# Kernel tuning notes

Hardware: AMD Instinct MI355X
Metric: run time of the kernel (lower is better)

The kernel has to match this reference:

```python
import jax, jax.numpy as jnp
import numpy as np

ROT_DELTA = 1  # rotation_delta from __init__
BN_EPS = 1e-3  # keras BatchNormalization default epsilon


def conv_dirac(signal, bc_idx, bc_w, W, b):
    """Template-based intrinsic mesh conv (dirac patch operator).

    signal: [N, D]; bc_idx/bc_w: [N, Rr, A, 3]; W: [T, Rr, A, D]; b: [T].
    Returns [N, K, T] with K = A // ROT_DELTA rotations.
    """
    gathered = signal[bc_idx]  # [N, Rr, A, 3, D] irregular gather
    interp = jnp.einsum('vrai,vraid->vrad', bc_w, gathered)  # barycentric interp
    A = interp.shape[2]
    rots = np.arange(0, A, ROT_DELTA)
    # Rotating the (small) template weights is equivalent to rolling the
    # interpolated signal along the angular axis, but far cheaper.
    W_rot = jnp.stack([jnp.roll(W, int(r), axis=2) for r in rots])  # [K, T, Rr, A, D]
    return jnp.einsum('vrad,ktrad->vkt', interp, W_rot) + b  # [N, K, T]


def angular_max_pool(x):
    # Select, per vertex, the rotation whose response has maximal L2 norm.
    k = jnp.argmax(jnp.linalg.norm(x, axis=-1), axis=1)  # [N]
    return jnp.take_along_axis(x, k[:, None, None], axis=1)[:, 0]  # [N, T]


def batch_norm(x, gamma, beta):
    mu = jnp.mean(x, axis=0, keepdims=True)
    var = jnp.var(x, axis=0, keepdims=True)
    return gamma * (x - mu) * jax.lax.rsqrt(var + BN_EPS) + beta


def setup_inputs() -> dict:
    key = jax.random.key(0)
    ks = jax.random.split(key, 6)
    N, Rr, A, D, T = 80000, 5, 8, 32, 32
    signal = jax.random.normal(ks[0], (N, D), dtype=jnp.float32)
    bc_idx = jax.random.randint(ks[1], (N, Rr, A, 3), 0, N)
    bc_w = jax.random.uniform(ks[2], (N, Rr, A, 3), dtype=jnp.float32)
    bc_w = bc_w / jnp.sum(bc_w, axis=-1, keepdims=True)  # barycentric coords sum to 1
    W1 = jax.random.normal(ks[3], (T, Rr, A, D), dtype=jnp.float32) * 0.05
    W2 = jax.random.normal(ks[4], (T, Rr, A, D), dtype=jnp.float32) * 0.05
    return {
        'signal': signal, 'bc_idx': bc_idx, 'bc_w': bc_w,
        'W1': W1, 'b1': jnp.zeros((T,), jnp.float32),
        'gamma1': jnp.ones((T,), jnp.float32), 'beta1': jnp.zeros((T,), jnp.float32),
        'W2': W2, 'b2': jnp.zeros((T,), jnp.float32),
        'gamma2': jnp.ones((T,), jnp.float32), 'beta2': jnp.zeros((T,), jnp.float32),
    }


def reference(signal, bc_idx, bc_w, W1, b1, gamma1, beta1, W2, b2, gamma2, beta2):
    # Branch 1: conv -> angular max-pool -> BN -> relu
    s = conv_dirac(signal, bc_idx, bc_w, W1, b1)
    s = angular_max_pool(s)
    s = batch_norm(s, gamma1, beta1)
    s = jax.nn.relu(s)
    # Branch 2: conv -> angular max-pool -> BN
    s = conv_dirac(s, bc_idx, bc_w, W2, b2)
    s = angular_max_pool(s)
    s = batch_norm(s, gamma2, beta2)
    # Residual add (input_dim == amt_templates -> no rescale branch) + activation
    return jax.nn.relu(s + signal)
```

## Files before the change

kernel.cpp:

```cpp
#include <hip/hip_runtime.h>
#include <math.h>

#define RR 5
#define AA 8
#define DD 32
#define TT 32
#define KK 8

#define RT2 0.70710678118654752f

typedef float v2f __attribute__((ext_vector_type(2)));
typedef float v4f __attribute__((ext_vector_type(4)));

static __device__ __forceinline__ v2f pkfma(v2f a, v2f b, v2f c) {
#if __has_builtin(__builtin_elementwise_fma)
    return __builtin_elementwise_fma(a, b, c);
#else
    v2f r; r.x = fmaf(a.x, b.x, c.x); r.y = fmaf(a.y, b.y, c.y); return r;
#endif
}

__global__ void wdft_kernel(const float* __restrict__ W, float* __restrict__ Ws) {
    int idx = blockIdx.x * 256 + threadIdx.x;
    if (idx >= TT * RR * DD) return;
    int d = idx & 31;
    int tr = idx >> 5;
    int t = tr / 5;
    int r = tr - t * 5;
    float xa[8];
    #pragma unroll
    for (int a = 0; a < 8; ++a) xa[a] = W[(tr * 8 + a) * 32 + d];
    float s0 = xa[0] + xa[4], d0 = xa[0] - xa[4];
    float s1 = xa[1] + xa[5], d1 = xa[1] - xa[5];
    float s2 = xa[2] + xa[6], d2 = xa[2] - xa[6];
    float s3 = xa[3] + xa[7], d3 = xa[3] - xa[7];
    float s02 = s0 + s2, s13 = s1 + s3;
    float F0 = s02 + s13, F4 = s02 - s13;
    float R2 = s0 - s2, I2 = s3 - s1;
    float u = RT2 * (d1 - d3), v = RT2 * (d1 + d3);
    float R1 = d0 + u, R3 = d0 - u;
    float I1 = -d2 - v, I3 = d2 - v;
    float* o = &Ws[(size_t)(((r * 32 + d) * 32 + t) * 8)];
    o[0] = F0; o[1] = F4; o[2] = R1; o[3] = I1;
    o[4] = R2; o[5] = I2; o[6] = R3; o[7] = I3;
}

__global__ __launch_bounds__(256, 2)
void fused_conv_kernel(const float* __restrict__ sig,
                       const int* __restrict__ bc_idx,
                       const float* __restrict__ bc_w,
                       const float* __restrict__ Wsg,
                       const float* __restrict__ bias,
                       float* __restrict__ s_out,
                       int N) {
    __shared__ float Is[64 * 260];
    __shared__ float Wl[8 * 260];

    int tid = threadIdx.x;
    int vBase = blockIdx.x * 64;
    int lane = tid & 63;
    int wv = tid >> 6;

    int vg = lane & 7;
    int tg = lane >> 3;
    int v0L = wv * 16 + vg * 2;
    int v0 = vBase + v0L;
    int v1 = v0 + 1;

    int d2 = tid & 15;
    int g = tid >> 4;

    v2f A0[2][4], A1[2][4], A2[2][4], A3[2][4];
    #pragma unroll
    for (int vv = 0; vv < 2; ++vv)
        #pragma unroll
        for (int j = 0; j < 4; ++j) {
            A0[vv][j] = (v2f){0.f, 0.f}; A1[vv][j] = (v2f){0.f, 0.f};
            A2[vv][j] = (v2f){0.f, 0.f}; A3[vv][j] = (v2f){0.f, 0.f};
        }

    const v2f rt2 = {RT2, RT2};
    const v4f* Ws4 = (const v4f*)Wsg;

    for (int r = 0; r < RR; ++r) {
        __syncthreads();

        #pragma unroll
        for (int vv0 = 0; vv0 < 4; ++vv0) {
            int vv = g + vv0 * 16;
            int vgl = vBase + vv;
            int vgc = (vgl < N) ? vgl : (N - 1);
            int base = (vgc * 40 + r * 8) * 3;
            v2f xa[8];
            #pragma unroll
            for (int a = 0; a < 8; ++a) {
                int i0 = bc_idx[base + a * 3 + 0];
                int i1 = bc_idx[base + a * 3 + 1];
                int i2 = bc_idx[base + a * 3 + 2];
                float w0 = bc_w[base + a * 3 + 0];
                float w1 = bc_w[base + a * 3 + 1];
                float w2 = bc_w[base + a * 3 + 2];
                v2f r0 = *(const v2f*)&sig[(size_t)i0 * 32 + 2 * d2];
                v2f r1 = *(const v2f*)&sig[(size_t)i1 * 32 + 2 * d2];
                v2f r2 = *(const v2f*)&sig[(size_t)i2 * 32 + 2 * d2];
                v2f w0v = {w0, w0};
                v2f w1v = {w1, w1};
                v2f w2v = {w2, w2};
                xa[a] = pkfma(w2v, r2, pkfma(w1v, r1, w0v * r0));
            }
            v2f s0 = xa[0] + xa[4], dd0 = xa[0] - xa[4];
            v2f s1 = xa[1] + xa[5], dd1 = xa[1] - xa[5];
            v2f s2 = xa[2] + xa[6], dd2 = xa[2] - xa[6];
            v2f s3 = xa[3] + xa[7], dd3 = xa[3] - xa[7];
            v2f s02 = s0 + s2, s13 = s1 + s3;
            v2f F0 = s02 + s13, F4 = s02 - s13;
            v2f R2 = s0 - s2, I2 = s3 - s1;
            v2f u = rt2 * (dd1 - dd3), vvv = rt2 * (dd1 + dd3);
            v2f R1 = dd0 + u, R3 = dd0 - u;
            v2f I1 = -dd2 - vvv, I3 = dd2 - vvv;
            float* ob = &Is[vv * 260 + (2 * d2) * 8];
            *(v4f*)&ob[0]  = (v4f){F0.x, F4.x, R1.x, I1.x};
            *(v4f*)&ob[4]  = (v4f){R2.x, I2.x, R3.x, I3.x};
            *(v4f*)&ob[8]  = (v4f){F0.y, F4.y, R1.y, I1.y};
            *(v4f*)&ob[12] = (v4f){R2.y, I2.y, R3.y, I3.y};
        }

        for (int ws = 0; ws < 4; ++ws) {
            __syncthreads();
            {
                const v4f* src = Ws4 + (size_t)(r * 32 + ws * 8) * 64;
                int dl = tid >> 5;
                int rem = (tid * 8) & 255;
                float* dst = &Wl[dl * 260 + rem];
                v4f a = src[tid * 2];
                v4f b = src[tid * 2 + 1];
                *(v4f*)dst = a;
                *(v4f*)(dst + 4) = b;
            }
            __syncthreads();

            #pragma unroll 2
            for (int dl = 0; dl < 8; ++dl) {
                int dg = ws * 8 + dl;
                const float* ip = &Is[v0L * 260 + dg * 8];
                v4f pa0 = *(const v4f*)&ip[0];
                v4f pb0 = *(const v4f*)&ip[4];
                v4f pa1 = *(const v4f*)&ip[260];
                v4f pb1 = *(const v4f*)&ip[264];
                v2f x1_0 = pa0.zw, x1n_0 = {pa0.w, -pa0.z};
                v2f x2_0 = pb0.xy, x2n_0 = {pb0.y, -pb0.x};
                v2f x3_0 = pb0.zw, x3n_0 = {pb0.w, -pb0.z};
                v2f x1_1 = pa1.zw, x1n_1 = {pa1.w, -pa1.z};
                v2f x2_1 = pb1.xy, x2n_1 = {pb1.y, -pb1.x};
                v2f x3_1 = pb1.zw, x3n_1 = {pb1.w, -pb1.z};
                const float* wrow = &Wl[dl * 260];
                #pragma unroll
                for (int j = 0; j < 4; ++j) {
                    v4f q0 = *(const v4f*)&wrow[(tg + 8 * j) * 8];
                    v4f q1 = *(const v4f*)&wrow[(tg + 8 * j) * 8 + 4];
                    v2f w2v = {q0.z, q0.z}, w3v = {q0.w, q0.w};
                    v2f w4v = {q1.x, q1.x}, w5v = {q1.y, q1.y};
                    v2f w6v = {q1.z, q1.z}, w7v = {q1.w, q1.w};
                    A0[0][j] = pkfma(pa0.xy, q0.xy, A0[0][j]);
                    A1[0][j] = pkfma(x1_0, w2v, A1[0][j]);
                    A1[0][j] = pkfma(x1n_0, w3v, A1[0][j]);
                    A2[0][j] = pkfma(x2_0, w4v, A2[0][j]);
                    A2[0][j] = pkfma(x2n_0, w5v, A2[0][j]);
                    A3[0][j] = pkfma(x3_0, w6v, A3[0][j]);
                    A3[0][j] = pkfma(x3n_0, w7v, A3[0][j]);
                    A0[1][j] = pkfma(pa1.xy, q0.xy, A0[1][j]);
                    A1[1][j] = pkfma(x1_1, w2v, A1[1][j]);
                    A1[1][j] = pkfma(x1n_1, w3v, A1[1][j]);
                    A2[1][j] = pkfma(x2_1, w4v, A2[1][j]);
                    A2[1][j] = pkfma(x2n_1, w5v, A2[1][j]);
                    A3[1][j] = pkfma(x3_1, w6v, A3[1][j]);
                    A3[1][j] = pkfma(x3n_1, w7v, A3[1][j]);
                }
            }
        }
    }

    float bj[4];
    #pragma unroll
    for (int j = 0; j < 4; ++j) bj[j] = bias[tg + 8 * j];

    float outk[2][8][4];
    #pragma unroll
    for (int vv = 0; vv < 2; ++vv) {
        #pragma unroll
        for (int j = 0; j < 4; ++j) {
            float C0 = A0[vv][j].x, C4 = A0[vv][j].y;
            float R1 = A1[vv][j].x, I1 = A1[vv][j].y;
            float R2 = A2[vv][j].x, I2 = A2[vv][j].y;
            float R3 = A3[vv][j].x, I3 = A3[vv][j].y;
            float e = 0.125f * (C0 + C4), o = 0.125f * (C0 - C4);
            float p = 0.25f * (R1 + R3), q = 0.25f * R2, s = 0.25f * (I1 - I3);
            float a_ = 0.25f * RT2 * (R1 - R3);
            float b_ = 0.25f * RT2 * (I1 + I3);
            float c_ = 0.25f * I2;
            float bb = bj[j];
            outk[vv][0][j] = e + p + q + bb;
            outk[vv][1][j] = o + a_ - b_ - c_ + bb;
            outk[vv][2][j] = e - s - q + bb;
            outk[vv][3][j] = o - a_ - b_ + c_ + bb;
            outk[vv][4][j] = e - p + q + bb;
            outk[vv][5][j] = o - a_ + b_ - c_ + bb;
            outk[vv][6][j] = e + s - q + bb;
            outk[vv][7][j] = o + a_ + b_ + c_ + bb;
        }
    }

    #pragma unroll
    for (int vv = 0; vv < 2; ++vv) {
        float norms[8];
        #pragma unroll
        for (int k = 0; k < 8; ++k) {
            float nl = 0.f;
            #pragma unroll
            for (int j = 0; j < 4; ++j)
                nl = fmaf(outk[vv][k][j], outk[vv][k][j], nl);
            nl += __shfl_xor(nl, 8);
            nl += __shfl_xor(nl, 16);
            nl += __shfl_xor(nl, 32);
            norms[k] = nl;
        }
        float best = -1.f;
        int bk = 0;
        #pragma unroll
        for (int k = 0; k < 8; ++k) {
            float n = sqrtf(norms[k]);
            if (n > best) { best = n; bk = k; }
        }
        int vOut = (vv == 0) ? v0 : v1;
        if (vOut < N) {
            float sel[4];
            #pragma unroll
            for (int j = 0; j < 4; ++j) sel[j] = 0.f;
            #pragma unroll
            for (int k = 0; k < 8; ++k) {
                if (k == bk) {
                    #pragma unroll
                    for (int j = 0; j < 4; ++j) sel[j] = outk[vv][k][j];
                }
            }
            float* o = s_out + (size_t)vOut * 32 + tg;
            o[0]  = sel[0];
            o[8]  = sel[1];
            o[16] = sel[2];
            o[24] = sel[3];
        }
    }
}

__global__ void stats_kernel(const float* __restrict__ s,
                             double* __restrict__ sums,
                             double* __restrict__ sumsq, int n) {
    __shared__ double la[256];
    __shared__ double lb[256];
    int tid = threadIdx.x;
    int t = tid & 31;
    int row = tid >> 5;
    double a = 0.0, b = 0.0;
    for (int v = blockIdx.x * 8 + row; v < n; v += gridDim.x * 8) {
        float x = s[(size_t)v * 32 + t];
        a += (double)x;
        b += (double)x * (double)x;
    }
    la[tid] = a; lb[tid] = b;
    __syncthreads();
    for (int off = 128; off >= 32; off >>= 1) {
        if (tid < off) { la[tid] += la[tid + off]; lb[tid] += lb[tid + off]; }
        __syncthreads();
    }
    if (tid < 32) {
        atomicAdd(&sums[t], la[tid]);
        atomicAdd(&sumsq[t], lb[tid]);
    }
}

__global__ void finalize_kernel(const double* __restrict__ sums,
                                const double* __restrict__ sumsq,
                                const float* __restrict__ gamma,
                                const float* __restrict__ beta,
                                float* __restrict__ scale,
                                float* __restrict__ shift, int n) {
    int t = threadIdx.x;
    if (t < 32) {
        double mu = sums[t] / (double)n;
        double var = sumsq[t] / (double)n - mu * mu;
        double sc = (double)gamma[t] / sqrt(var + 1e-3);
        scale[t] = (float)sc;
        shift[t] = (float)((double)beta[t] - mu * sc);
    }
}

__global__ void affine_relu_kernel(const float* __restrict__ s,
                                   const float* __restrict__ scale,
                                   const float* __restrict__ shift,
                                   float* __restrict__ o, int n4) {
    int e = blockIdx.x * blockDim.x + threadIdx.x;
    if (e >= n4) return;
    int t0 = (e & 7) * 4;
    float4 x = ((const float4*)s)[e];
    float4 y;
    y.x = fmaxf(fmaf(scale[t0 + 0], x.x, shift[t0 + 0]), 0.f);
    y.y = fmaxf(fmaf(scale[t0 + 1], x.y, shift[t0 + 1]), 0.f);
    y.z = fmaxf(fmaf(scale[t0 + 2], x.z, shift[t0 + 2]), 0.f);
    y.w = fmaxf(fmaf(scale[t0 + 3], x.w, shift[t0 + 3]), 0.f);
    ((float4*)o)[e] = y;
}

__global__ void final_kernel(const float* __restrict__ s,
                             const float* __restrict__ scale,
                             const float* __restrict__ shift,
                             const float* __restrict__ sig,
                             float* __restrict__ o, int n4) {
    int e = blockIdx.x * blockDim.x + threadIdx.x;
    if (e >= n4) return;
    int t0 = (e & 7) * 4;
    float4 x = ((const float4*)s)[e];
    float4 z = ((const float4*)sig)[e];
    float4 y;
    y.x = fmaxf(fmaf(scale[t0 + 0], x.x, shift[t0 + 0]) + z.x, 0.f);
    y.y = fmaxf(fmaf(scale[t0 + 1], x.y, shift[t0 + 1]) + z.y, 0.f);
    y.z = fmaxf(fmaf(scale[t0 + 2], x.z, shift[t0 + 2]) + z.z, 0.f);
    y.w = fmaxf(fmaf(scale[t0 + 3], x.w, shift[t0 + 3]) + z.w, 0.f);
    ((float4*)o)[e] = y;
}

__global__ void zero_stats_kernel(double* __restrict__ d, float* __restrict__ f) {
    int t = threadIdx.x;
    if (t < 128) d[t] = 0.0;
    if (t < 128) f[t] = 0.f;
}

extern "C" void kernel_launch(void* const* d_in, const int* in_sizes, int n_in,
                              void* d_out, int out_size, void* d_ws, size_t ws_size,
                              hipStream_t stream) {
    const float* signal = (const float*)d_in[0];
    const int* bc_idx   = (const int*)d_in[1];
    const float* bc_w   = (const float*)d_in[2];
    const float* W1     = (const float*)d_in[3];
    const float* b1     = (const float*)d_in[4];
    const float* g1     = (const float*)d_in[5];
    const float* be1    = (const float*)d_in[6];
    const float* W2     = (const float*)d_in[7];
    const float* b2     = (const float*)d_in[8];
    const float* g2     = (const float*)d_in[9];
    const float* be2    = (const float*)d_in[10];
    float* out = (float*)d_out;

    const int N = in_sizes[0] / 32;

    char* ws = (char*)d_ws;
    double* sums1  = (double*)ws;
    double* sumsq1 = sums1 + 32;
    double* sums2  = sums1 + 64;
    double* sumsq2 = sums1 + 96;
    float* scale1 = (float*)(ws + 1024);
    float* shift1 = scale1 + 32;
    float* scale2 = scale1 + 64;
    float* shift2 = scale1 + 96;
    float* Ws1 = (float*)(ws + 4096);
    float* Ws2 = Ws1 + RR * DD * TT * 8;
    float* s1  = Ws2 + RR * DD * TT * 8;
    float* sg2 = s1 + (size_t)N * 32;
    float* s2  = sg2 + (size_t)N * 32;

    int nBlocks = (N + 63) / 64;
    int wBlocks = (TT * RR * DD + 255) / 256;

    zero_stats_kernel<<<1, 128, 0, stream>>>((double*)ws, (float*)(ws + 1024));
    wdft_kernel<<<wBlocks, 256, 0, stream>>>(W1, Ws1);
    wdft_kernel<<<wBlocks, 256, 0, stream>>>(W2, Ws2);

    fused_conv_kernel<<<nBlocks, 256, 0, stream>>>(signal, bc_idx, bc_w, Ws1, b1, s1, N);
    stats_kernel<<<64, 256, 0, stream>>>(s1, sums1, sumsq1, N);
    finalize_kernel<<<1, 32, 0, stream>>>(sums1, sumsq1, g1, be1, scale1, shift1, N);
    affine_relu_kernel<<<(N * 8 + 255) / 256, 256, 0, stream>>>(s1, scale1, shift1, sg2, N * 8);

    fused_conv_kernel<<<nBlocks, 256, 0, stream>>>(sg2, bc_idx, bc_w, Ws2, b2, s2, N);
    stats_kernel<<<64, 256, 0, stream>>>(s2, sums2, sumsq2, N);
    finalize_kernel<<<1, 32, 0, stream>>>(sums2, sumsq2, g2, be2, scale2, shift2, N);

    final_kernel<<<(N * 8 + 255) / 256, 256, 0, stream>>>(s2, scale2, shift2, signal, out, N * 8);
}
```

Before: 713.5 us.

## Fuse BN statistics into conv kernel, widen gathers, merge prep kernels

BatchNorm sum and sum-of-squares are now computed in the conv kernel's epilogue using wave shuffles, an LDS reduction and double atomics, which removes the separate stats kernel and its re-read of the conv output. The gather stage now uses 4-wide signal loads, and barycentric indices and weights are loaded as int4/float4 vectors. The weight DFT layout is changed to allow unpadded contiguous LDS rows. The zeroing and the two weight-DFT launches are merged into one prep kernel. Risks are atomic contention from 1250 blocks per channel and a different vertex-to-thread mapping that may change LDS bank conflicts.

```diff
diff --git a/kernel.cpp b/kernel.cpp
--- a/kernel.cpp
+++ b/kernel.cpp
@@ -19,9 +19,27 @@
     v2f r; r.x = fmaf(a.x, b.x, c.x); r.y = fmaf(a.y, b.y, c.y); return r;
 #endif
 }
-
-__global__ void wdft_kernel(const float* __restrict__ W, float* __restrict__ Ws) {
-    int idx = blockIdx.x * 256 + threadIdx.x;
+static __device__ __forceinline__ v4f pkfma4(v4f a, v4f b, v4f c) {
+#if __has_builtin(__builtin_elementwise_fma)
+    return __builtin_elementwise_fma(a, b, c);
+#else
+    v4f r;
+    r.x = fmaf(a.x, b.x, c.x); r.y = fmaf(a.y, b.y, c.y);
+    r.z = fmaf(a.z, b.z, c.z); r.w = fmaf(a.w, b.w, c.w);
+    return r;
+#endif
+}
+
+__global__ void prep_kernel(const float* __restrict__ W1, const float* __restrict__ W2,
+                            float* __restrict__ Ws1, float* __restrict__ Ws2,
+                            double* __restrict__ dz, float* __restrict__ fz) {
+    int b = blockIdx.x;
+    int tid = threadIdx.x;
+    if (b == 0 && tid < 128) { dz[tid] = 0.0; fz[tid] = 0.f; }
+    int which = (b >= 20) ? 1 : 0;
+    const float* __restrict__ W = which ? W2 : W1;
+    float* __restrict__ Ws = which ? Ws2 : Ws1;
+    int idx = (b - which * 20) * 256 + tid;
     if (idx >= TT * RR * DD) return;
     int d = idx & 31;
     int tr = idx >> 5;
@@ -40,9 +58,9 @@
     float u = RT2 * (d1 - d3), v = RT2 * (d1 + d3);
     float R1 = d0 + u, R3 = d0 - u;
     float I1 = -d2 - v, I3 = d2 - v;
-    float* o = &Ws[(size_t)(((r * 32 + d) * 32 + t) * 8)];
-    o[0] = F0; o[1] = F4; o[2] = R1; o[3] = I1;
-    o[4] = R2; o[5] = I2; o[6] = R3; o[7] = I3;
+    float* o = &Ws[(size_t)(r * 32 + d) * 256];
+    *(v4f*)&o[t * 4]       = (v4f){F0, F4, R1, I1};
+    *(v4f*)&o[128 + t * 4] = (v4f){R2, I2, R3, I3};
 }
 
 __global__ __launch_bounds__(256, 2)
@@ -52,9 +70,11 @@
                        const float* __restrict__ Wsg,
                        const float* __restrict__ bias,
                        float* __restrict__ s_out,
+                       double* __restrict__ sums,
+                       double* __restrict__ sumsq,
                        int N) {
     __shared__ float Is[64 * 260];
-    __shared__ float Wl[8 * 260];
+    __shared__ float Wl[8 * 256];
 
     int tid = threadIdx.x;
     int vBase = blockIdx.x * 64;
@@ -63,12 +83,13 @@
 
     int vg = lane & 7;
     int tg = lane >> 3;
-    int v0L = wv * 16 + vg * 2;
+    int v0L = wv * 16 + vg;
+    int v1L = v0L + 8;
     int v0 = vBase + v0L;
-    int v1 = v0 + 1;
-
-    int d2 = tid & 15;
-    int g = tid >> 4;
+    int v1 = vBase + v1L;
+
+    int d4 = tid & 7;
+    int g = tid >> 3;
 
     v2f A0[2][4], A1[2][4], A2[2][4], A3[2][4];
     #pragma unroll
@@ -79,59 +100,65 @@
             A2[vv][j] = (v2f){0.f, 0.f}; A3[vv][j] = (v2f){0.f, 0.f};
         }
 
-    const v2f rt2 = {RT2, RT2};
     const v4f* Ws4 = (const v4f*)Wsg;
 
     for (int r = 0; r < RR; ++r) {
         __syncthreads();
 
         #pragma unroll
-        for (int vv0 = 0; vv0 < 4; ++vv0) {
-            int vv = g + vv0 * 16;
+        for (int vv0 = 0; vv0 < 2; ++vv0) {
+            int vv = g + vv0 * 32;
             int vgl = vBase + vv;
             int vgc = (vgl < N) ? vgl : (N - 1);
-            int base = (vgc * 40 + r * 8) * 3;
-            v2f xa[8];
+            int base = vgc * 120 + r * 24;
+            int idxv[24]; float wbc[24];
+            const int4* ib = (const int4*)(bc_idx + base);
+            const float4* fb = (const float4*)(bc_w + base);
+            #pragma unroll
+            for (int q = 0; q < 6; ++q) {
+                *(int4*)&idxv[q * 4] = ib[q];
+                *(float4*)&wbc[q * 4] = fb[q];
+            }
+            v4f xa[8];
             #pragma unroll
             for (int a = 0; a < 8; ++a) {
-                int i0 = bc_idx[base + a * 3 + 0];
-                int i1 = bc_idx[base + a * 3 + 1];
-                int i2 = bc_idx[base + a * 3 + 2];
-                float w0 = bc_w[base + a * 3 + 0];
-                float w1 = bc_w[base + a * 3 + 1];
-                float w2 = bc_w[base + a * 3 + 2];
-                v2f r0 = *(const v2f*)&sig[(size_t)i0 * 32 + 2 * d2];
-                v2f r1 = *(const v2f*)&sig[(size_t)i1 * 32 + 2 * d2];
-                v2f r2 = *(const v2f*)&sig[(size_t)i2 * 32 + 2 * d2];
-                v2f w0v = {w0, w0};
-                v2f w1v = {w1, w1};
-                v2f w2v = {w2, w2};
-                xa[a] = pkfma(w2v, r2, pkfma(w1v, r1, w0v * r0));
-            }
-            v2f s0 = xa[0] + xa[4], dd0 = xa[0] - xa[4];
-            v2f s1 = xa[1] + xa[5], dd1 = xa[1] - xa[5];
-            v2f s2 = xa[2] + xa[6], dd2 = xa[2] - xa[6];
-            v2f s3 = xa[3] + xa[7], dd3 = xa[3] - xa[7];
-            v2f s02 = s0 + s2, s13 = s1 + s3;
-            v2f F0 = s02 + s13, F4 = s02 - s13;
-            v2f R2 = s0 - s2, I2 = s3 - s1;
-            v2f u = rt2 * (dd1 - dd3), vvv = rt2 * (dd1 + dd3);
-            v2f R1 = dd0 + u, R3 = dd0 - u;
-            v2f I1 = -dd2 - vvv, I3 = dd2 - vvv;
-            float* ob = &Is[vv * 260 + (2 * d2) * 8];
-            *(v4f*)&ob[0]  = (v4f){F0.x, F4.x, R1.x, I1.x};
-            *(v4f*)&ob[4]  = (v4f){R2.x, I2.x, R3.x, I3.x};
-            *(v4f*)&ob[8]  = (v4f){F0.y, F4.y, R1.y, I1.y};
-            *(v4f*)&ob[12] = (v4f){R2.y, I2.y, R3.y, I3.y};
+                int i0 = idxv[a * 3 + 0];
+                int i1 = idxv[a * 3 + 1];
+                int i2 = idxv[a * 3 + 2];
+                v4f r0 = *(const v4f*)&sig[(size_t)i0 * 32 + 4 * d4];
+                v4f r1 = *(const v4f*)&sig[(size_t)i1 * 32 + 4 * d4];
+                v4f r2 = *(const v4f*)&sig[(size_t)i2 * 32 + 4 * d4];
+                float w0 = wbc[a * 3 + 0];
+                float w1 = wbc[a * 3 + 1];
+                float w2 = wbc[a * 3 + 2];
+                v4f w0v = (v4f){w0, w0, w0, w0};
+                v4f w1v = (v4f){w1, w1, w1, w1};
+                v4f w2v = (v4f){w2, w2, w2, w2};
+                xa[a] = pkfma4(w2v, r2, pkfma4(w1v, r1, w0v * r0));
+            }
+            v4f s0 = xa[0] + xa[4], dd0 = xa[0] - xa[4];
+            v4f s1 = xa[1] + xa[5], dd1 = xa[1] - xa[5];
+            v4f s2 = xa[2] + xa[6], dd2 = xa[2] - xa[6];
+            v4f s3 = xa[3] + xa[7], dd3 = xa[3] - xa[7];
+            v4f s02 = s0 + s2, s13 = s1 + s3;
+            v4f F0 = s02 + s13, F4 = s02 - s13;
+            v4f R2 = s0 - s2, I2 = s3 - s1;
+            v4f u = RT2 * (dd1 - dd3), vt = RT2 * (dd1 + dd3);
+            v4f R1 = dd0 + u, R3 = dd0 - u;
+            v4f I1 = -dd2 - vt, I3 = dd2 - vt;
+            float* ob = &Is[vv * 260 + d4 * 32];
+            #pragma unroll
+            for (int di = 0; di < 4; ++di) {
+                *(v4f*)&ob[di * 8]     = (v4f){F0[di], F4[di], R1[di], I1[di]};
+                *(v4f*)&ob[di * 8 + 4] = (v4f){R2[di], I2[di], R3[di], I3[di]};
+            }
         }
 
         for (int ws = 0; ws < 4; ++ws) {
             __syncthreads();
             {
                 const v4f* src = Ws4 + (size_t)(r * 32 + ws * 8) * 64;
-                int dl = tid >> 5;
-                int rem = (tid * 8) & 255;
-                float* dst = &Wl[dl * 260 + rem];
+                float* dst = &Wl[tid * 8];
                 v4f a = src[tid * 2];
                 v4f b = src[tid * 2 + 1];
                 *(v4f*)dst = a;
@@ -141,23 +168,22 @@
 
             #pragma unroll 2
             for (int dl = 0; dl < 8; ++dl) {
-                int dg = ws * 8 + dl;
-                const float* ip = &Is[v0L * 260 + dg * 8];
+                const float* ip = &Is[v0L * 260 + (ws * 8 + dl) * 8];
                 v4f pa0 = *(const v4f*)&ip[0];
                 v4f pb0 = *(const v4f*)&ip[4];
-                v4f pa1 = *(const v4f*)&ip[260];
-                v4f pb1 = *(const v4f*)&ip[264];
+                v4f pa1 = *(const v4f*)&ip[2080];
+                v4f pb1 = *(const v4f*)&ip[2084];
                 v2f x1_0 = pa0.zw, x1n_0 = {pa0.w, -pa0.z};
                 v2f x2_0 = pb0.xy, x2n_0 = {pb0.y, -pb0.x};
                 v2f x3_0 = pb0.zw, x3n_0 = {pb0.w, -pb0.z};
                 v2f x1_1 = pa1.zw, x1n_1 = {pa1.w, -pa1.z};
                 v2f x2_1 = pb1.xy, x2n_1 = {pb1.y, -pb1.x};
                 v2f x3_1 = pb1.zw, x3n_1 = {pb1.w, -pb1.z};
-                const float* wrow = &Wl[dl * 260];
+                const float* wrow = &Wl[dl * 256];
                 #pragma unroll
                 for (int j = 0; j < 4; ++j) {
-                    v4f q0 = *(const v4f*)&wrow[(tg + 8 * j) * 8];
-                    v4f q1 = *(const v4f*)&wrow[(tg + 8 * j) * 8 + 4];
+                    v4f q0 = *(const v4f*)&wrow[(tg + 8 * j) * 4];
+                    v4f q1 = *(const v4f*)&wrow[(tg + 8 * j) * 4 + 128];
                     v2f w2v = {q0.z, q0.z}, w3v = {q0.w, q0.w};
                     v2f w4v = {q1.x, q1.x}, w5v = {q1.y, q1.y};
                     v2f w6v = {q1.z, q1.z}, w7v = {q1.w, q1.w};
@@ -210,6 +236,8 @@
         }
     }
 
+    float sel[2][4];
+    int vOutA[2]; vOutA[0] = v0; vOutA[1] = v1;
     #pragma unroll
     for (int vv = 0; vv < 2; ++vv) {
         float norms[8];
@@ -231,50 +259,59 @@
             float n = sqrtf(norms[k]);
             if (n > best) { best = n; bk = k; }
         }
-        int vOut = (vv == 0) ? v0 : v1;
-        if (vOut < N) {
-            float sel[4];
-            #pragma unroll
-            for (int j = 0; j < 4; ++j) sel[j] = 0.f;
-            #pragma unroll
-            for (int k = 0; k < 8; ++k) {
-                if (k == bk) {
-                    #pragma unroll
-                    for (int j = 0; j < 4; ++j) sel[j] = outk[vv][k][j];
-                }
-            }
-            float* o = s_out + (size_t)vOut * 32 + tg;
-            o[0]  = sel[0];
-            o[8]  = sel[1];
-            o[16] = sel[2];
-            o[24] = sel[3];
-        }
-    }
-}
-
-__global__ void stats_kernel(const float* __restrict__ s,
-                             double* __restrict__ sums,
-                             double* __restrict__ sumsq, int n) {
-    __shared__ double la[256];
-    __shared__ double lb[256];
-    int tid = threadIdx.x;
-    int t = tid & 31;
-    int row = tid >> 5;
-    double a = 0.0, b = 0.0;
-    for (int v = blockIdx.x * 8 + row; v < n; v += gridDim.x * 8) {
-        float x = s[(size_t)v * 32 + t];
-        a += (double)x;
-        b += (double)x * (double)x;
-    }
-    la[tid] = a; lb[tid] = b;
+        #pragma unroll
+        for (int j = 0; j < 4; ++j) sel[vv][j] = 0.f;
+        #pragma unroll
+        for (int k = 0; k < 8; ++k) {
+            if (k == bk) {
+                #pragma unroll
+                for (int j = 0; j < 4; ++j) sel[vv][j] = outk[vv][k][j];
+            }
+        }
+        if (vOutA[vv] < N) {
+            float* o = s_out + (size_t)vOutA[vv] * 32 + tg;
+            o[0]  = sel[vv][0];
+            o[8]  = sel[vv][1];
+            o[16] = sel[vv][2];
+            o[24] = sel[vv][3];
+        }
+    }
+
+    float pa_[4], pb_[4];
+    #pragma unroll
+    for (int j = 0; j < 4; ++j) {
+        float s0 = (v0 < N) ? sel[0][j] : 0.f;
+        float s1 = (v1 < N) ? sel[1][j] : 0.f;
+        pa_[j] = s0 + s1;
+        pb_[j] = fmaf(s0, s0, s1 * s1);
+    }
+    #pragma unroll
+    for (int j = 0; j < 4; ++j) {
+        pa_[j] += __shfl_xor(pa_[j], 1);
+        pb_[j] += __shfl_xor(pb_[j], 1);
+        pa_[j] += __shfl_xor(pa_[j], 2);
+        pb_[j] += __shfl_xor(pb_[j], 2);
+        pa_[j] += __shfl_xor(pa_[j], 4);
+        pb_[j] += __shfl_xor(pb_[j], 4);
+    }
     __syncthreads();
-    for (int off = 128; off >= 32; off >>= 1) {
-        if (tid < off) { la[tid] += la[tid + off]; lb[tid] += lb[tid + off]; }
-        __syncthreads();
-    }
-    if (tid < 32) {
-        atomicAdd(&sums[t], la[tid]);
-        atomicAdd(&sumsq[t], lb[tid]);
+    if (vg == 0) {
+        float* wst = (float*)Wl;
+        #pragma unroll
+        for (int j = 0; j < 4; ++j) {
+            int t = tg + 8 * j;
+            wst[(wv * 32 + t) * 2 + 0] = pa_[j];
+            wst[(wv * 32 + t) * 2 + 1] = pb_[j];
+        }
+    }
+    __syncthreads();
+    if (tid < 64) {
+        const float* wst = (const float*)Wl;
+        int t = tid >> 1, c = tid & 1;
+        float s = wst[t * 2 + c] + wst[64 + t * 2 + c] +
+                  wst[128 + t * 2 + c] + wst[192 + t * 2 + c];
+        if (c == 0) atomicAdd(&sums[t], (double)s);
+        else        atomicAdd(&sumsq[t], (double)s);
     }
 }
 
@@ -328,12 +365,6 @@
     ((float4*)o)[e] = y;
 }
 
-__global__ void zero_stats_kernel(double* __restrict__ d, float* __restrict__ f) {
-    int t = threadIdx.x;
-    if (t < 128) d[t] = 0.0;
-    if (t < 128) f[t] = 0.f;
-}
-
 extern "C" void kernel_launch(void* const* d_in, const int* in_sizes, int n_in,
                               void* d_out, int out_size, void* d_ws, size_t ws_size,
                               hipStream_t stream) {
@@ -368,19 +399,16 @@
     float* s2  = sg2 + (size_t)N * 32;
 
     int nBlocks = (N + 63) / 64;
-    int wBlocks = (TT * RR * DD + 255) / 256;
-
-    zero_stats_kernel<<<1, 128, 0, stream>>>((double*)ws, (float*)(ws + 1024));
-    wdft_kernel<<<wBlocks, 256, 0, stream>>>(W1, Ws1);
-    wdft_kernel<<<wBlocks, 256, 0, stream>>>(W2, Ws2);
-
-    fused_conv_kernel<<<nBlocks, 256, 0, stream>>>(signal, bc_idx, bc_w, Ws1, b1, s1, N);
-    stats_kernel<<<64, 256, 0, stream>>>(s1, sums1, sumsq1, N);
+
+    prep_kernel<<<40, 256, 0, stream>>>(W1, W2, Ws1, Ws2, (double*)ws, (float*)(ws + 1024));
+
+    fused_conv_kernel<<<nBlocks, 256, 0, stream>>>(signal, bc_idx, bc_w, Ws1, b1, s1,
+                                                   sums1, sumsq1, N);
     finalize_kernel<<<1, 32, 0, stream>>>(sums1, sumsq1, g1, be1, scale1, shift1, N);
     affine_relu_kernel<<<(N * 8 + 255) / 256, 256, 0, stream>>>(s1, scale1, shift1, sg2, N * 8);
 
-    fused_conv_kernel<<<nBlocks, 256, 0, stream>>>(sg2, bc_idx, bc_w, Ws2, b2, s2, N);
-    stats_kernel<<<64, 256, 0, stream>>>(s2, sums2, sumsq2, N);
+    fused_conv_kernel<<<nBlocks, 256, 0, stream>>>(sg2, bc_idx, bc_w, Ws2, b2, s2,
+                                                   sums2, sumsq2, N);
     finalize_kernel<<<1, 32, 0, stream>>>(sums2, sumsq2, g2, be2, scale2, shift2, N);
 
     final_kernel<<<(N * 8 + 255) / 256, 256, 0, stream>>>(s2, scale2, shift2, signal, out, N * 8);
```

After: 627.4 us. -12.1%, faster.
